# Kernel tuning notes

Hardware: AMD Instinct MI355X
Metric: run time of the kernel (lower is better)

## Reference

```python
import jax, jax.numpy as jnp
import numpy as np

B, T, I, U, O, BB = 256, 1024, 64, 256, 64, 128  # batch, seq, input, units, output, backbone_units

def lecun_tanh(x):
    return 1.7159 * jnp.tanh(0.666 * x)

def setup_inputs() -> dict:
    key = jax.random.key(0)
    ks = jax.random.split(key, 13)
    def lin(k, fan_in, fan_out):
        bound = 1.0 / np.sqrt(fan_in)
        kw, kb = jax.random.split(k)
        W = jax.random.uniform(kw, (fan_in, fan_out), jnp.float32, -bound, bound)
        b = jax.random.uniform(kb, (fan_out,), jnp.float32, -bound, bound)
        return W, b
    x = jax.random.normal(ks[0], (B, T, I), jnp.float32)
    W_bb, b_bb = lin(ks[1], I + U, BB)   # backbone Linear
    W_ff1, b_ff1 = lin(ks[2], BB, U)
    W_ff2, b_ff2 = lin(ks[3], BB, U)
    W_ta, b_ta = lin(ks[4], BB, U)       # time_a
    W_tb, b_tb = lin(ks[5], BB, U)       # time_b
    W_fc, b_fc = lin(ks[6], U, O)        # readout
    return {"x": x, "W_bb": W_bb, "b_bb": b_bb, "W_ff1": W_ff1, "b_ff1": b_ff1,
            "W_ff2": W_ff2, "b_ff2": b_ff2, "W_ta": W_ta, "b_ta": b_ta,
            "W_tb": W_tb, "b_tb": b_tb, "W_fc": W_fc, "b_fc": b_fc}

def reference(x, W_bb, b_bb, W_ff1, b_ff1, W_ff2, b_ff2, W_ta, b_ta, W_tb, b_tb, W_fc, b_fc):
    ts = jnp.float32(1.0)  # default elapsed time per step
    def step(h, xt):
        z = jnp.concatenate([xt, h], axis=-1)          # [B, I+U]
        g = lecun_tanh(z @ W_bb + b_bb)                # [B, BB]
        ff1 = jnp.tanh(g @ W_ff1 + b_ff1)              # [B, U]
        ff2 = jnp.tanh(g @ W_ff2 + b_ff2)
        t_interp = jax.nn.sigmoid((g @ W_ta + b_ta) * ts + (g @ W_tb + b_tb))
        h_new = ff1 * (1.0 - t_interp) + t_interp * ff2
        return h_new, h_new
    h0 = jnp.zeros((x.shape[0], U), x.dtype)
    h_last, hs = jax.lax.scan(step, h0, jnp.swapaxes(x, 0, 1))  # hs: [T, B, U]
    hs = jnp.swapaxes(hs, 0, 1)                                  # [B, T, U]
    out = hs @ W_fc + b_fc                                       # [B, T, O]
    return out, h_last
```

## Files before the change

### kernel.cpp

```cpp
#include <hip/hip_runtime.h>
#include <stdint.h>

#define B_ 256
#define T_ 1024
#define I_ 64
#define U_ 256
#define O_ 64
#define BB_ 128

typedef unsigned int u32;
typedef unsigned short u16;
typedef _Float16 half2_t __attribute__((ext_vector_type(2)));
typedef _Float16 f16x8 __attribute__((ext_vector_type(8)));
typedef float f32x4 __attribute__((ext_vector_type(4)));

#if defined(__has_builtin)
#if __has_builtin(__builtin_amdgcn_fdot2)
#define USE_DOT2 1
#else
#define USE_DOT2 0
#endif
#else
#define USE_DOT2 0
#endif

static __device__ __forceinline__ u32 packpair(float a, float b) {
  half2_t h; h.x = (_Float16)a; h.y = (_Float16)b;
  return __builtin_bit_cast(u32, h);
}
static __device__ __forceinline__ float unpack_lo(u32 u) {
  half2_t h = __builtin_bit_cast(half2_t, u); return (float)h.x;
}
static __device__ __forceinline__ float unpack_hi(u32 u) {
  half2_t h = __builtin_bit_cast(half2_t, u); return (float)h.y;
}
static __device__ __forceinline__ float dot2acc(u32 w, u32 z, float acc) {
#if USE_DOT2
  return __builtin_amdgcn_fdot2(__builtin_bit_cast(half2_t, w),
                                __builtin_bit_cast(half2_t, z), acc, false);
#else
  half2_t hw = __builtin_bit_cast(half2_t, w);
  half2_t hz = __builtin_bit_cast(half2_t, z);
  acc += (float)hw.x * (float)hz.x;
  acc += (float)hw.y * (float)hz.y;
  return acc;
#endif
}

template <int CTRL>
static __device__ __forceinline__ float dpp_mov_f(float v) {
  return __builtin_bit_cast(float, __builtin_amdgcn_update_dpp(
      0, __builtin_bit_cast(int, v), CTRL, 0xF, 0xF, true));
}
#define DPP_XOR1 0xB1
#define DPP_XOR2 0x4E
#define DPP_HMIR 0x141
#define DPP_MIRR 0x140

static __device__ __forceinline__ float fast_tanh(float x) {
  return 1.0f - 2.0f / (1.0f + __expf(2.0f * x));
}
static __device__ __forceinline__ float fast_sigmoid(float x) {
  return 1.0f / (1.0f + __expf(-x));
}

static __device__ __forceinline__ float rcpf(float x) {
#if defined(__has_builtin) && __has_builtin(__builtin_amdgcn_rcpf)
  return __builtin_amdgcn_rcpf(x);
#else
  return 1.0f / x;
#endif
}
static __device__ __forceinline__ float exp2fast(float x) {
#if defined(__has_builtin) && __has_builtin(__builtin_amdgcn_exp2f)
  return __builtin_amdgcn_exp2f(x);
#else
  return exp2f(x);
#endif
}

static __device__ __forceinline__ f32x4 mfma16(uint4 a, uint4 b, f32x4 c) {
  return __builtin_amdgcn_mfma_f32_16x16x32_f16(
      __builtin_bit_cast(f16x8, a), __builtin_bit_cast(f16x8, b), c, 0, 0, 0);
}

static __device__ __forceinline__ void wg_barrier() {
  asm volatile("s_waitcnt lgkmcnt(0)\n\ts_barrier" ::: "memory");
}

static __device__ __forceinline__ int swzw(int w) {
  return w ^ ((w >> 4) & 4);
}

#define LOG2E 1.44269504f

__global__ __launch_bounds__(512, 2)
void cfc_mfma(const float* __restrict__ x,
              const float* __restrict__ W_bb, const float* __restrict__ b_bb,
              const float* __restrict__ W_ff1, const float* __restrict__ b_ff1,
              const float* __restrict__ W_ff2, const float* __restrict__ b_ff2,
              const float* __restrict__ W_ta,  const float* __restrict__ b_ta,
              const float* __restrict__ W_tb,  const float* __restrict__ b_tb,
              float* __restrict__ out, u32* __restrict__ Hbuf)
{
  __shared__ __align__(16) u32 s_z[2560];
  __shared__ __align__(16) u32 s_g[1024];

  const int tid = threadIdx.x;
  const int l   = tid & 63;
  const int w   = tid >> 6;
  const int c16 = l & 15;
  const int q4  = l >> 4;
  const int odd = l & 1;
  const int row0 = blockIdx.x * 16;
  const int lr = l ^ ((l >> 4) & 1);

  uint4 wbb[10];
  {
    const int colb = w * 16 + c16;
#pragma unroll
    for (int c = 0; c < 10; ++c) {
      u32 qv[4];
#pragma unroll
      for (int q = 0; q < 4; ++q) {
        const int k0 = c * 32 + q4 * 8 + 2 * q;
        qv[q] = packpair(W_bb[(size_t)k0 * BB_ + colb],
                         W_bb[(size_t)(k0 + 1) * BB_ + colb]);
      }
      wbb[c] = make_uint4(qv[0], qv[1], qv[2], qv[3]);
    }
  }
  uint4 wff[3][2][4];
#pragma unroll
  for (int ut = 0; ut < 2; ++ut) {
    const int u = w * 32 + ut * 16 + c16;
#pragma unroll
    for (int c = 0; c < 4; ++c) {
      u32 qa[4], qb[4], qc[4];
#pragma unroll
      for (int q = 0; q < 4; ++q) {
        const int k0 = c * 32 + q4 * 8 + 2 * q;
        const size_t i0 = (size_t)k0 * U_ + u, i1 = i0 + U_;
        qa[q] = packpair(W_ff1[i0], W_ff1[i1]);
        qb[q] = packpair(W_ff2[i0], W_ff2[i1]);
        qc[q] = packpair(W_ta[i0] + W_tb[i0], W_ta[i1] + W_tb[i1]);
      }
      wff[0][ut][c] = make_uint4(qa[0], qa[1], qa[2], qa[3]);
      wff[1][ut][c] = make_uint4(qb[0], qb[1], qb[2], qb[3]);
      wff[2][ut][c] = make_uint4(qc[0], qc[1], qc[2], qc[3]);
    }
  }

  const float bgs = b_bb[w * 16 + c16] * (1.332f * LOG2E);
  float b1s[2], b2s[2], btn[2];
#pragma unroll
  for (int ut = 0; ut < 2; ++ut) {
    const int u = w * 32 + ut * 16 + c16;
    b1s[ut] = b_ff1[u] * (2.0f * LOG2E);
    b2s[ut] = b_ff2[u] * (2.0f * LOG2E);
    btn[ut] = -(b_ta[u] + b_tb[u]) * LOG2E;
  }

  const int mx = tid >> 5, px = tid & 31;
  const float* xptr = x + (size_t)(row0 + mx) * T_ * I_ + 2 * px;
  const int zxs = swzw(((px >> 4) * 64 + mx + 16 * ((px >> 2) & 3)) * 4 + (px & 3));

  const int rbase = odd ? 2 : 0;
  const int m0 = q4 * 4 + rbase, m1 = m0 + 1;
  const int pg = w * 8 + (c16 >> 1);
  const int gW = ((pg >> 4) * 64 + 16 * ((pg >> 2) & 3)) * 4 + (pg & 3)
                 + 16 * q4 + (odd ? 8 : 0);
  const int gws0 = swzw(gW), gws1 = swzw(gW + 4);
  int zws0_[2], zws1_[2]; size_t hb0_[2], hb1_[2];
#pragma unroll
  for (int ut = 0; ut < 2; ++ut) {
    const int pu = w * 16 + ut * 8 + (c16 >> 1);
    const int zW = ((2 + (pu >> 4)) * 64 + 16 * ((pu >> 2) & 3)) * 4 + (pu & 3)
                   + 16 * q4 + (odd ? 8 : 0);
    zws0_[ut] = swzw(zW);
    zws1_[ut] = swzw(zW + 4);
    hb0_[ut] = (size_t)(row0 + m0) * T_ * 128 + pu;
    hb1_[ut] = (size_t)(row0 + m1) * T_ * 128 + pu;
  }

  {
    uint4* z4w = reinterpret_cast<uint4*>(s_z);
#pragma unroll
    for (int i = tid; i < 640; i += 512) z4w[i] = make_uint4(0u, 0u, 0u, 0u);
  }
  __syncthreads();
  {
    float2 xv = *(const float2*)xptr;
    s_z[zxs] = packpair(xv.x, xv.y);
  }
  __syncthreads();

  const uint4* z4 = (const uint4*)s_z;
  const uint4* g4 = (const uint4*)s_g;

  for (int t = 0; t < T_; ++t) {
    float2 xv;
    const bool ldx = (t + 1 < T_);
    if (ldx) xv = *(const float2*)(xptr + (size_t)(t + 1) * I_);

    f32x4 aA = {0.f, 0.f, 0.f, 0.f}, aB = {0.f, 0.f, 0.f, 0.f};
#pragma unroll
    for (int c = 0; c < 10; c += 2) {
      aA = mfma16(z4[c * 64 + lr],       wbb[c],     aA);
      aB = mfma16(z4[(c + 1) * 64 + lr], wbb[c + 1], aB);
    }
    const f32x4 ab = aA + aB;

    u32 gq[4];
#pragma unroll
    for (int r = 0; r < 4; ++r) {
      const float a  = __builtin_fmaf(ab[r], 1.332f * LOG2E, bgs);
      const float rr = rcpf(exp2fast(a) + 1.0f);
      const float g  = __builtin_fmaf(rr, -3.4318f, 1.7159f);
      const float gp = dpp_mov_f<DPP_XOR1>(g);
      gq[r] = odd ? packpair(gp, g) : packpair(g, gp);
    }
    s_g[gws0] = odd ? gq[2] : gq[0];
    s_g[gws1] = odd ? gq[3] : gq[1];
    wg_barrier();

    f32x4 af[3][2];
#pragma unroll
    for (int mt = 0; mt < 3; ++mt)
#pragma unroll
      for (int ut = 0; ut < 2; ++ut)
        af[mt][ut] = (f32x4){0.f, 0.f, 0.f, 0.f};
#pragma unroll
    for (int c = 0; c < 4; ++c) {
      const uint4 ga = g4[c * 64 + lr];
#pragma unroll
      for (int mt = 0; mt < 3; ++mt)
#pragma unroll
        for (int ut = 0; ut < 2; ++ut)
          af[mt][ut] = mfma16(ga, wff[mt][ut][c], af[mt][ut]);
    }

#pragma unroll
    for (int ut = 0; ut < 2; ++ut) {
      u32 hq[4];
#pragma unroll
      for (int r = 0; r < 4; ++r) {
        const float a1 = __builtin_fmaf(af[0][ut][r], 2.0f * LOG2E, b1s[ut]);
        const float f1 = __builtin_fmaf(rcpf(exp2fast(a1) + 1.0f), -2.0f, 1.0f);
        const float a2 = __builtin_fmaf(af[1][ut][r], 2.0f * LOG2E, b2s[ut]);
        const float f2 = __builtin_fmaf(rcpf(exp2fast(a2) + 1.0f), -2.0f, 1.0f);
        const float at = __builtin_fmaf(af[2][ut][r], -LOG2E, btn[ut]);
        const float ti = rcpf(exp2fast(at) + 1.0f);
        const float h  = __builtin_fmaf(ti, f2 - f1, f1);
        const float hp = dpp_mov_f<DPP_XOR1>(h);
        hq[r] = odd ? packpair(hp, h) : packpair(h, hp);
      }
      const u32 s0 = odd ? hq[2] : hq[0];
      const u32 s1 = odd ? hq[3] : hq[1];
      s_z[zws0_[ut]] = s0;
      s_z[zws1_[ut]] = s1;
      Hbuf[hb0_[ut] + (size_t)t * 128] = s0;
      Hbuf[hb1_[ut] + (size_t)t * 128] = s1;
    }
    if (ldx) s_z[zxs] = packpair(xv.x, xv.y);
    wg_barrier();
  }

  {
    const uint4 hv = z4[128 + (tid ^ ((tid >> 4) & 1))];
    float2* tail = (float2*)(out + (size_t)B_ * T_ * O_);
#pragma unroll
    for (int i = 0; i < 4; ++i) {
      const int vh   = tid * 4 + i;
      const int ch   = vh >> 8;
      const int lane = (vh >> 2) & 63;
      const int slot = vh & 3;
      const int m    = lane & 15;
      const int bq   = lane >> 4;
      const int pu   = ch * 16 + bq * 4 + slot;
      const u32 hp   = (i == 0) ? hv.x : (i == 1) ? hv.y : (i == 2) ? hv.z : hv.w;
      float2 hf; hf.x = unpack_lo(hp); hf.y = unpack_hi(hp);
      tail[(size_t)(row0 + m) * 128 + pu] = hf;
    }
  }
}

template <bool DEFER>
__global__ __launch_bounds__(1024)
void cfc_kernel(const float* __restrict__ x,
                const float* __restrict__ W_bb, const float* __restrict__ b_bb,
                const float* __restrict__ W_ff1, const float* __restrict__ b_ff1,
                const float* __restrict__ W_ff2, const float* __restrict__ b_ff2,
                const float* __restrict__ W_ta,  const float* __restrict__ b_ta,
                const float* __restrict__ W_tb,  const float* __restrict__ b_tb,
                const float* __restrict__ W_fc,  const float* __restrict__ b_fc,
                float* __restrict__ out, u32* __restrict__ Hbuf)
{
  __shared__ __align__(16) u32 s_z2[160];
  __shared__ __align__(16) u32 s_g2[64];
  u16* s_gh = (u16*)s_g2;

  const int tid = threadIdx.x;
  const int r   = blockIdx.x;

  const int ca  = tid >> 3;
  const int kga = tid & 7;
  const int jb = tid >> 2;
  const int kq = tid & 3;
  const int ro = tid >> 4;
  const int rk = tid & 15;

  u32 wbb[20];
#pragma unroll
  for (int j = 0; j < 5; ++j)
#pragma unroll
    for (int q = 0; q < 4; ++q) {
      int p = 4 * (kga + 8 * j) + q;
      wbb[4 * j + q] = packpair(W_bb[(2 * p) * BB_ + ca],
                                W_bb[(2 * p + 1) * BB_ + ca]);
    }
  u32 wf1[16], wf2[16], wta[16], wtb[16];
#pragma unroll
  for (int j = 0; j < 4; ++j)
#pragma unroll
    for (int q = 0; q < 4; ++q) {
      int p = 4 * (kq + 4 * j) + q;
      int k0 = 2 * p, k1 = 2 * p + 1;
      wf1[4 * j + q] = packpair(W_ff1[k0 * U_ + jb], W_ff1[k1 * U_ + jb]);
      wf2[4 * j + q] = packpair(W_ff2[k0 * U_ + jb], W_ff2[k1 * U_ + jb]);
      wta[4 * j + q] = packpair(W_ta [k0 * U_ + jb], W_ta [k1 * U_ + jb]);
      wtb[4 * j + q] = packpair(W_tb [k0 * U_ + jb], W_tb [k1 * U_ + jb]);
    }
  u32 wfc[8];
  float bfo = 0.f;
  if (!DEFER) {
#pragma unroll
    for (int j = 0; j < 2; ++j)
#pragma unroll
      for (int q = 0; q < 4; ++q) {
        int p = 4 * (rk + 16 * j) + q;
        wfc[4 * j + q] = packpair(W_fc[(2 * p) * O_ + ro],
                                  W_fc[(2 * p + 1) * O_ + ro]);
      }
    bfo = b_fc[ro];
  }
  const float bbbc = b_bb[ca];
  const float b1 = b_ff1[jb], b2 = b_ff2[jb];
  const float bta = b_ta[jb], btb = b_tb[jb];

  const float* xrow = x + (size_t)r * T_ * I_;
  const size_t out_row = (size_t)r * T_ * O_;
  u32* __restrict__ hrow = DEFER ? (Hbuf + (size_t)r * T_ * (U_ / 2)) : nullptr;

  if (tid < 160) s_z2[tid] = 0u;
  __syncthreads();
  if (tid < 32) {
    float2 xv = ((const float2*)xrow)[tid];
    s_z2[tid] = packpair(xv.x, xv.y);
  }
  __syncthreads();

  for (int t = 0; t < T_; ++t) {
    float2 xv;
    const bool ldx = (tid < 32) && (t + 1 < T_);
    if (ldx) xv = ((const float2*)(xrow + (size_t)(t + 1) * I_))[tid];

    float bacc = 0.f;
#pragma unroll
    for (int j = 0; j < 5; ++j) {
      uint4 zz = *reinterpret_cast<const uint4*>(s_z2 + 4 * (kga + 8 * j));
      bacc = dot2acc(wbb[4 * j + 0], zz.x, bacc);
      bacc = dot2acc(wbb[4 * j + 1], zz.y, bacc);
      bacc = dot2acc(wbb[4 * j + 2], zz.z, bacc);
      bacc = dot2acc(wbb[4 * j + 3], zz.w, bacc);
    }
    bacc += dpp_mov_f<DPP_XOR1>(bacc);
    bacc += dpp_mov_f<DPP_XOR2>(bacc);
    bacc += dpp_mov_f<DPP_HMIR>(bacc);
    float g = 1.7159f * fast_tanh(0.666f * (bacc + bbbc));

    float racc = 0.f;
    if (!DEFER) {
#pragma unroll
      for (int j = 0; j < 2; ++j) {
        uint4 hh = *reinterpret_cast<const uint4*>(s_z2 + 32 + 4 * (rk + 16 * j));
        racc = dot2acc(wfc[4 * j + 0], hh.x, racc);
        racc = dot2acc(wfc[4 * j + 1], hh.y, racc);
        racc = dot2acc(wfc[4 * j + 2], hh.z, racc);
        racc = dot2acc(wfc[4 * j + 3], hh.w, racc);
      }
      racc += dpp_mov_f<DPP_XOR1>(racc);
      racc += dpp_mov_f<DPP_XOR2>(racc);
      racc += dpp_mov_f<DPP_HMIR>(racc);
      racc += dpp_mov_f<DPP_MIRR>(racc);
    }
    if ((tid & 7) == 0)
      s_gh[ca] = __builtin_bit_cast(u16, (_Float16)g);
    if (!DEFER && t > 0 && rk == 0)
      out[out_row + (size_t)(t - 1) * O_ + ro] = racc + bfo;
    __syncthreads();

    float a1 = 0.f, a2 = 0.f, a3 = 0.f, a4 = 0.f;
#pragma unroll
    for (int j = 0; j < 4; ++j) {
      uint4 gg = *reinterpret_cast<const uint4*>(s_g2 + 4 * (kq + 4 * j));
      a1 = dot2acc(wf1[4 * j + 0], gg.x, a1);
      a1 = dot2acc(wf1[4 * j + 1], gg.y, a1);
      a1 = dot2acc(wf1[4 * j + 2], gg.z, a1);
      a1 = dot2acc(wf1[4 * j + 3], gg.w, a1);
      a2 = dot2acc(wf2[4 * j + 0], gg.x, a2);
      a2 = dot2acc(wf2[4 * j + 1], gg.y, a2);
      a2 = dot2acc(wf2[4 * j + 2], gg.z, a2);
      a2 = dot2acc(wf2[4 * j + 3], gg.w, a2);
      a3 = dot2acc(wta[4 * j + 0], gg.x, a3);
      a3 = dot2acc(wta[4 * j + 1], gg.y, a3);
      a3 = dot2acc(wta[4 * j + 2], gg.z, a3);
      a3 = dot2acc(wta[4 * j + 3], gg.w, a3);
      a4 = dot2acc(wtb[4 * j + 0], gg.x, a4);
      a4 = dot2acc(wtb[4 * j + 1], gg.y, a4);
      a4 = dot2acc(wtb[4 * j + 2], gg.z, a4);
      a4 = dot2acc(wtb[4 * j + 3], gg.w, a4);
    }
    a1 += dpp_mov_f<DPP_XOR1>(a1); a1 += dpp_mov_f<DPP_XOR2>(a1);
    a2 += dpp_mov_f<DPP_XOR1>(a2); a2 += dpp_mov_f<DPP_XOR2>(a2);
    a3 += dpp_mov_f<DPP_XOR1>(a3); a3 += dpp_mov_f<DPP_XOR2>(a3);
    a4 += dpp_mov_f<DPP_XOR1>(a4); a4 += dpp_mov_f<DPP_XOR2>(a4);
    float f1 = fast_tanh(a1 + b1);
    float f2 = fast_tanh(a2 + b2);
    float ti = fast_sigmoid(a3 + bta + a4 + btb);
    float h  = f1 + ti * (f2 - f1);
    float hq = dpp_mov_f<DPP_HMIR>(h);

    if ((tid & 7) == 0) {
      u32 pr = packpair(h, hq);
      int m = tid >> 3;
      s_z2[32 + m] = pr;
      if (DEFER) hrow[(size_t)t * (U_ / 2) + m] = pr;
    }
    if (ldx) s_z2[tid] = packpair(xv.x, xv.y);
    __syncthreads();
  }

  if (!DEFER) {
    float racc = 0.f;
#pragma unroll
    for (int j = 0; j < 2; ++j) {
      uint4 hh = *reinterpret_cast<const uint4*>(s_z2 + 32 + 4 * (rk + 16 * j));
      racc = dot2acc(wfc[4 * j + 0], hh.x, racc);
      racc = dot2acc(wfc[4 * j + 1], hh.y, racc);
      racc = dot2acc(wfc[4 * j + 2], hh.z, racc);
      racc = dot2acc(wfc[4 * j + 3], hh.w, racc);
    }
    racc += dpp_mov_f<DPP_XOR1>(racc);
    racc += dpp_mov_f<DPP_XOR2>(racc);
    racc += dpp_mov_f<DPP_HMIR>(racc);
    racc += dpp_mov_f<DPP_MIRR>(racc);
    if (rk == 0)
      out[out_row + (size_t)(T_ - 1) * O_ + ro] = racc + bfo;
  }

  if (tid < 128) {
    u32 hp = s_z2[32 + tid];
    float2 hv; hv.x = unpack_lo(hp); hv.y = unpack_hi(hp);
    ((float2*)(out + (size_t)B_ * T_ * O_))[r * 128 + tid] = hv;
  }
}

__global__ __launch_bounds__(512)
void ro_kernel(const u32* __restrict__ Hbuf,
               const float* __restrict__ W_fc, const float* __restrict__ b_fc,
               float* __restrict__ out)
{
  __shared__ __align__(16) u32 s_h[8 * 128];
  const int tid = threadIdx.x;
  const int o   = tid & 63;
  const int w   = tid >> 6;
  const int r   = blockIdx.x;

  u32 wfc[128];
#pragma unroll
  for (int p = 0; p < 128; ++p)
    wfc[p] = packpair(W_fc[(2 * p) * O_ + o], W_fc[(2 * p + 1) * O_ + o]);
  const float bo = b_fc[o];

  const u32* hrow = Hbuf + (size_t)r * T_ * 128;
  const size_t out_row = (size_t)r * T_ * O_;

  for (int c = 0; c < T_ / 8; ++c) {
    *(uint2*)(s_h + 2 * tid) =
        *(const uint2*)(hrow + (size_t)c * 1024 + 2 * tid);
    __syncthreads();
    float acc = bo;
    const uint4* h4 = reinterpret_cast<const uint4*>(s_h + w * 128);
#pragma unroll
    for (int i = 0; i < 32; ++i) {
      uint4 hh = h4[i];
      acc = dot2acc(wfc[4 * i + 0], hh.x, acc);
      acc = dot2acc(wfc[4 * i + 1], hh.y, acc);
      acc = dot2acc(wfc[4 * i + 2], hh.z, acc);
      acc = dot2acc(wfc[4 * i + 3], hh.w, acc);
    }
    out[out_row + (size_t)(8 * c + w) * O_ + o] = acc;
    __syncthreads();
  }
}

extern "C" void kernel_launch(void* const* d_in, const int* in_sizes, int n_in,
                              void* d_out, int out_size, void* d_ws, size_t ws_size,
                              hipStream_t stream) {
  const float* x     = (const float*)d_in[0];
  const float* W_bb  = (const float*)d_in[1];
  const float* b_bb  = (const float*)d_in[2];
  const float* W_ff1 = (const float*)d_in[3];
  const float* b_ff1 = (const float*)d_in[4];
  const float* W_ff2 = (const float*)d_in[5];
  const float* b_ff2 = (const float*)d_in[6];
  const float* W_ta  = (const float*)d_in[7];
  const float* b_ta  = (const float*)d_in[8];
  const float* W_tb  = (const float*)d_in[9];
  const float* b_tb  = (const float*)d_in[10];
  const float* W_fc  = (const float*)d_in[11];
  const float* b_fc  = (const float*)d_in[12];
  float* out = (float*)d_out;

  const size_t h_bytes = (size_t)B_ * T_ * (U_ / 2) * sizeof(u32);
  if (ws_size >= h_bytes) {
    u32* Hbuf = (u32*)d_ws;
    cfc_mfma<<<dim3(B_ / 16), dim3(512), 0, stream>>>(
        x, W_bb, b_bb, W_ff1, b_ff1, W_ff2, b_ff2,
        W_ta, b_ta, W_tb, b_tb, out, Hbuf);
    ro_kernel<<<dim3(B_), dim3(512), 0, stream>>>(Hbuf, W_fc, b_fc, out);
  } else {
    cfc_kernel<false><<<dim3(B_), dim3(1024), 0, stream>>>(
        x, W_bb, b_bb, W_ff1, b_ff1, W_ff2, b_ff2,
        W_ta, b_ta, W_tb, b_tb, W_fc, b_fc, out, nullptr);
  }
}
```

Before: 1.946 ms.

## Split recurrent step across 16 waves with split-K backbone and parallel readout

The recurrent kernel moves from 8 to 16 waves per block. The backbone matmul is split in K across two wave groups, with the partial sums reduced through shared memory, and each wave now handles one 16-unit output tile instead of two. The gate math is rewritten to use a single reciprocal per element instead of three, and the readout kernel grid is split over time chunks to get more blocks. The aim is to shorten the per-step serial latency of the 16-block recurrence, at the cost of an extra barrier per step and fewer register-resident weights per wave.

```diff
diff --git a/kernel.cpp b/kernel.cpp
--- a/kernel.cpp
+++ b/kernel.cpp
@@ -94,7 +94,7 @@
 
 #define LOG2E 1.44269504f
 
-__global__ __launch_bounds__(512, 2)
+__global__ __launch_bounds__(1024, 4)
 void cfc_mfma(const float* __restrict__ x,
               const float* __restrict__ W_bb, const float* __restrict__ b_bb,
               const float* __restrict__ W_ff1, const float* __restrict__ b_ff1,
@@ -105,93 +105,85 @@
 {
   __shared__ __align__(16) u32 s_z[2560];
   __shared__ __align__(16) u32 s_g[1024];
+  __shared__ __align__(16) float s_red[2048];
 
   const int tid = threadIdx.x;
   const int l   = tid & 63;
   const int w   = tid >> 6;
+  const int wt  = w & 7;
+  const int kh  = w >> 3;
   const int c16 = l & 15;
   const int q4  = l >> 4;
   const int odd = l & 1;
   const int row0 = blockIdx.x * 16;
-  const int lr = l ^ ((l >> 4) & 1);
-
-  uint4 wbb[10];
+  const int lr  = l ^ ((l >> 4) & 1);
+
+  uint4 wbb[5];
   {
-    const int colb = w * 16 + c16;
-#pragma unroll
-    for (int c = 0; c < 10; ++c) {
+    const int colb = wt * 16 + c16;
+#pragma unroll
+    for (int c = 0; c < 5; ++c) {
+      const int kc = kh * 5 + c;
       u32 qv[4];
 #pragma unroll
       for (int q = 0; q < 4; ++q) {
-        const int k0 = c * 32 + q4 * 8 + 2 * q;
+        const int k0 = kc * 32 + q4 * 8 + 2 * q;
         qv[q] = packpair(W_bb[(size_t)k0 * BB_ + colb],
                          W_bb[(size_t)(k0 + 1) * BB_ + colb]);
       }
       wbb[c] = make_uint4(qv[0], qv[1], qv[2], qv[3]);
     }
   }
-  uint4 wff[3][2][4];
-#pragma unroll
-  for (int ut = 0; ut < 2; ++ut) {
-    const int u = w * 32 + ut * 16 + c16;
-#pragma unroll
-    for (int c = 0; c < 4; ++c) {
-      u32 qa[4], qb[4], qc[4];
-#pragma unroll
-      for (int q = 0; q < 4; ++q) {
-        const int k0 = c * 32 + q4 * 8 + 2 * q;
-        const size_t i0 = (size_t)k0 * U_ + u, i1 = i0 + U_;
-        qa[q] = packpair(W_ff1[i0], W_ff1[i1]);
-        qb[q] = packpair(W_ff2[i0], W_ff2[i1]);
-        qc[q] = packpair(W_ta[i0] + W_tb[i0], W_ta[i1] + W_tb[i1]);
-      }
-      wff[0][ut][c] = make_uint4(qa[0], qa[1], qa[2], qa[3]);
-      wff[1][ut][c] = make_uint4(qb[0], qb[1], qb[2], qb[3]);
-      wff[2][ut][c] = make_uint4(qc[0], qc[1], qc[2], qc[3]);
-    }
-  }
-
-  const float bgs = b_bb[w * 16 + c16] * (1.332f * LOG2E);
-  float b1s[2], b2s[2], btn[2];
-#pragma unroll
-  for (int ut = 0; ut < 2; ++ut) {
-    const int u = w * 32 + ut * 16 + c16;
-    b1s[ut] = b_ff1[u] * (2.0f * LOG2E);
-    b2s[ut] = b_ff2[u] * (2.0f * LOG2E);
-    btn[ut] = -(b_ta[u] + b_tb[u]) * LOG2E;
-  }
-
-  const int mx = tid >> 5, px = tid & 31;
+  uint4 wff0[4], wff1[4], wff2[4];
+  const int uu = w * 16 + c16;
+#pragma unroll
+  for (int c = 0; c < 4; ++c) {
+    u32 qa[4], qb[4], qc[4];
+#pragma unroll
+    for (int q = 0; q < 4; ++q) {
+      const int k0 = c * 32 + q4 * 8 + 2 * q;
+      const size_t i0 = (size_t)k0 * U_ + uu, i1 = i0 + U_;
+      qa[q] = packpair(W_ff1[i0], W_ff1[i1]);
+      qb[q] = packpair(W_ff2[i0], W_ff2[i1]);
+      qc[q] = packpair(W_ta[i0] + W_tb[i0], W_ta[i1] + W_tb[i1]);
+    }
+    wff0[c] = make_uint4(qa[0], qa[1], qa[2], qa[3]);
+    wff1[c] = make_uint4(qb[0], qb[1], qb[2], qb[3]);
+    wff2[c] = make_uint4(qc[0], qc[1], qc[2], qc[3]);
+  }
+
+  const float bgs = b_bb[wt * 16 + c16] * (1.332f * LOG2E);
+  const float b1s = b_ff1[uu] * (2.0f * LOG2E);
+  const float b2s = b_ff2[uu] * (2.0f * LOG2E);
+  const float btn = -(b_ta[uu] + b_tb[uu]) * LOG2E;
+
+  const int ix = tid & 511;
+  const int mx = ix >> 5, px = ix & 31;
   const float* xptr = x + (size_t)(row0 + mx) * T_ * I_ + 2 * px;
-  const int zxs = swzw(((px >> 4) * 64 + mx + 16 * ((px >> 2) & 3)) * 4 + (px & 3));
-
-  const int rbase = odd ? 2 : 0;
-  const int m0 = q4 * 4 + rbase, m1 = m0 + 1;
-  const int pg = w * 8 + (c16 >> 1);
-  const int gW = ((pg >> 4) * 64 + 16 * ((pg >> 2) & 3)) * 4 + (pg & 3)
-                 + 16 * q4 + (odd ? 8 : 0);
+  const int zxs = swzw((px >> 4) * 256 + 64 * ((px >> 2) & 3) + 4 * mx + (px & 3));
+
+  const int m0 = 4 * q4 + 2 * odd;
+  const int pg = wt * 8 + (c16 >> 1);
+  const int gW = (pg >> 4) * 256 + 64 * ((pg >> 2) & 3) + (pg & 3) + 4 * m0;
   const int gws0 = swzw(gW), gws1 = swzw(gW + 4);
-  int zws0_[2], zws1_[2]; size_t hb0_[2], hb1_[2];
-#pragma unroll
-  for (int ut = 0; ut < 2; ++ut) {
-    const int pu = w * 16 + ut * 8 + (c16 >> 1);
-    const int zW = ((2 + (pu >> 4)) * 64 + 16 * ((pu >> 2) & 3)) * 4 + (pu & 3)
-                   + 16 * q4 + (odd ? 8 : 0);
-    zws0_[ut] = swzw(zW);
-    zws1_[ut] = swzw(zW + 4);
-    hb0_[ut] = (size_t)(row0 + m0) * T_ * 128 + pu;
-    hb1_[ut] = (size_t)(row0 + m1) * T_ * 128 + pu;
-  }
+
+  const int pu = w * 8 + (c16 >> 1);
+  const int pz = 32 + pu;
+  const int zW = (pz >> 4) * 256 + 64 * ((pz >> 2) & 3) + (pz & 3) + 4 * m0;
+  const int zws0 = swzw(zW), zws1 = swzw(zW + 4);
+  const u32 hoff0 = (u32)(row0 + m0) * T_ * 128 + pu;
+  const u32 hoff1 = hoff0 + (u32)T_ * 128;
+
+  const int redw = (wt * 64 + l) * 4;
 
   {
     uint4* z4w = reinterpret_cast<uint4*>(s_z);
-#pragma unroll
-    for (int i = tid; i < 640; i += 512) z4w[i] = make_uint4(0u, 0u, 0u, 0u);
+    if (tid < 640) z4w[tid] = make_uint4(0u, 0u, 0u, 0u);
   }
   __syncthreads();
-  {
-    float2 xv = *(const float2*)xptr;
-    s_z[zxs] = packpair(xv.x, xv.y);
+  if (w >= 8) {
+    float2 x0 = *(const float2*)xptr;
+    s_z[zxs] = packpair(x0.x, x0.y);
   }
   __syncthreads();
 
@@ -200,73 +192,76 @@
 
   for (int t = 0; t < T_; ++t) {
     float2 xv;
-    const bool ldx = (t + 1 < T_);
+    const bool ldx = (w >= 8) && (t + 1 < T_);
     if (ldx) xv = *(const float2*)(xptr + (size_t)(t + 1) * I_);
 
     f32x4 aA = {0.f, 0.f, 0.f, 0.f}, aB = {0.f, 0.f, 0.f, 0.f};
-#pragma unroll
-    for (int c = 0; c < 10; c += 2) {
-      aA = mfma16(z4[c * 64 + lr],       wbb[c],     aA);
-      aB = mfma16(z4[(c + 1) * 64 + lr], wbb[c + 1], aB);
+    {
+      const int cb = kh * 5;
+      aA = mfma16(z4[(cb + 0) * 64 + lr], wbb[0], aA);
+      aB = mfma16(z4[(cb + 1) * 64 + lr], wbb[1], aB);
+      aA = mfma16(z4[(cb + 2) * 64 + lr], wbb[2], aA);
+      aB = mfma16(z4[(cb + 3) * 64 + lr], wbb[3], aB);
+      aA = mfma16(z4[(cb + 4) * 64 + lr], wbb[4], aA);
     }
     const f32x4 ab = aA + aB;
-
-    u32 gq[4];
-#pragma unroll
-    for (int r = 0; r < 4; ++r) {
-      const float a  = __builtin_fmaf(ab[r], 1.332f * LOG2E, bgs);
-      const float rr = rcpf(exp2fast(a) + 1.0f);
-      const float g  = __builtin_fmaf(rr, -3.4318f, 1.7159f);
-      const float gp = dpp_mov_f<DPP_XOR1>(g);
-      gq[r] = odd ? packpair(gp, g) : packpair(g, gp);
-    }
-    s_g[gws0] = odd ? gq[2] : gq[0];
-    s_g[gws1] = odd ? gq[3] : gq[1];
+    if (kh) *(f32x4*)(s_red + redw) = ab;
     wg_barrier();
 
-    f32x4 af[3][2];
-#pragma unroll
-    for (int mt = 0; mt < 3; ++mt)
-#pragma unroll
-      for (int ut = 0; ut < 2; ++ut)
-        af[mt][ut] = (f32x4){0.f, 0.f, 0.f, 0.f};
+    if (!kh) {
+      const f32x4 pr = *(const f32x4*)(s_red + redw);
+      u32 gq[4];
+#pragma unroll
+      for (int r = 0; r < 4; ++r) {
+        const float full = ab[r] + pr[r];
+        const float a  = __builtin_fmaf(full, 1.332f * LOG2E, bgs);
+        const float rr = rcpf(exp2fast(a) + 1.0f);
+        const float g  = __builtin_fmaf(rr, -3.4318f, 1.7159f);
+        const float gp = dpp_mov_f<DPP_XOR1>(g);
+        gq[r] = odd ? packpair(gp, g) : packpair(g, gp);
+      }
+      s_g[gws0] = odd ? gq[2] : gq[0];
+      s_g[gws1] = odd ? gq[3] : gq[1];
+    }
+    wg_barrier();
+
+    f32x4 af0 = {0.f, 0.f, 0.f, 0.f};
+    f32x4 af1 = {0.f, 0.f, 0.f, 0.f};
+    f32x4 af2 = {0.f, 0.f, 0.f, 0.f};
 #pragma unroll
     for (int c = 0; c < 4; ++c) {
       const uint4 ga = g4[c * 64 + lr];
-#pragma unroll
-      for (int mt = 0; mt < 3; ++mt)
-#pragma unroll
-        for (int ut = 0; ut < 2; ++ut)
-          af[mt][ut] = mfma16(ga, wff[mt][ut][c], af[mt][ut]);
-    }
-
-#pragma unroll
-    for (int ut = 0; ut < 2; ++ut) {
-      u32 hq[4];
-#pragma unroll
-      for (int r = 0; r < 4; ++r) {
-        const float a1 = __builtin_fmaf(af[0][ut][r], 2.0f * LOG2E, b1s[ut]);
-        const float f1 = __builtin_fmaf(rcpf(exp2fast(a1) + 1.0f), -2.0f, 1.0f);
-        const float a2 = __builtin_fmaf(af[1][ut][r], 2.0f * LOG2E, b2s[ut]);
-        const float f2 = __builtin_fmaf(rcpf(exp2fast(a2) + 1.0f), -2.0f, 1.0f);
-        const float at = __builtin_fmaf(af[2][ut][r], -LOG2E, btn[ut]);
-        const float ti = rcpf(exp2fast(at) + 1.0f);
-        const float h  = __builtin_fmaf(ti, f2 - f1, f1);
-        const float hp = dpp_mov_f<DPP_XOR1>(h);
-        hq[r] = odd ? packpair(hp, h) : packpair(h, hp);
-      }
-      const u32 s0 = odd ? hq[2] : hq[0];
-      const u32 s1 = odd ? hq[3] : hq[1];
-      s_z[zws0_[ut]] = s0;
-      s_z[zws1_[ut]] = s1;
-      Hbuf[hb0_[ut] + (size_t)t * 128] = s0;
-      Hbuf[hb1_[ut] + (size_t)t * 128] = s1;
+      af0 = mfma16(ga, wff0[c], af0);
+      af1 = mfma16(ga, wff1[c], af1);
+      af2 = mfma16(ga, wff2[c], af2);
     }
     if (ldx) s_z[zxs] = packpair(xv.x, xv.y);
+
+    u32 hq[4];
+#pragma unroll
+    for (int r = 0; r < 4; ++r) {
+      const float E1 = exp2fast(__builtin_fmaf(af0[r], 2.0f * LOG2E, b1s));
+      const float E2 = exp2fast(__builtin_fmaf(af1[r], 2.0f * LOG2E, b2s));
+      const float E3 = exp2fast(__builtin_fmaf(af2[r], -LOG2E, btn));
+      const float p2 = E2 + 1.0f, p3 = E3 + 1.0f;
+      const float qq = p2 * p3;
+      const float D  = __builtin_fmaf(E1, qq, qq);
+      const float R  = rcpf(D);
+      const float u2 = (E2 - E1) - qq;
+      const float h  = __builtin_fmaf(R + R, u2, 1.0f);
+      const float hp = dpp_mov_f<DPP_XOR1>(h);
+      hq[r] = odd ? packpair(hp, h) : packpair(h, hp);
+    }
+    const u32 s0 = odd ? hq[2] : hq[0];
+    const u32 s1 = odd ? hq[3] : hq[1];
+    s_z[zws0] = s0;
+    s_z[zws1] = s1;
+    Hbuf[hoff0 + (u32)t * 128] = s0;
+    Hbuf[hoff1 + (u32)t * 128] = s1;
     wg_barrier();
   }
 
-  {
+  if (tid < 512) {
     const uint4 hv = z4[128 + (tid ^ ((tid >> 4) & 1))];
     float2* tail = (float2*)(out + (size_t)B_ * T_ * O_);
 #pragma unroll
@@ -277,10 +272,10 @@
       const int slot = vh & 3;
       const int m    = lane & 15;
       const int bq   = lane >> 4;
-      const int pu   = ch * 16 + bq * 4 + slot;
+      const int pp   = ch * 16 + bq * 4 + slot;
       const u32 hp   = (i == 0) ? hv.x : (i == 1) ? hv.y : (i == 2) ? hv.z : hv.w;
       float2 hf; hf.x = unpack_lo(hp); hf.y = unpack_hi(hp);
-      tail[(size_t)(row0 + m) * 128 + pu] = hf;
+      tail[(size_t)(row0 + m) * 128 + pp] = hf;
     }
   }
 }
@@ -476,6 +471,7 @@
   const int o   = tid & 63;
   const int w   = tid >> 6;
   const int r   = blockIdx.x;
+  const int c0  = blockIdx.y * 16;
 
   u32 wfc[128];
 #pragma unroll
@@ -486,7 +482,7 @@
   const u32* hrow = Hbuf + (size_t)r * T_ * 128;
   const size_t out_row = (size_t)r * T_ * O_;
 
-  for (int c = 0; c < T_ / 8; ++c) {
+  for (int c = c0; c < c0 + 16; ++c) {
     *(uint2*)(s_h + 2 * tid) =
         *(const uint2*)(hrow + (size_t)c * 1024 + 2 * tid);
     __syncthreads();
@@ -526,10 +522,10 @@
   const size_t h_bytes = (size_t)B_ * T_ * (U_ / 2) * sizeof(u32);
   if (ws_size >= h_bytes) {
     u32* Hbuf = (u32*)d_ws;
-    cfc_mfma<<<dim3(B_ / 16), dim3(512), 0, stream>>>(
+    cfc_mfma<<<dim3(B_ / 16), dim3(1024), 0, stream>>>(
         x, W_bb, b_bb, W_ff1, b_ff1, W_ff2, b_ff2,
         W_ta, b_ta, W_tb, b_tb, out, Hbuf);
-    ro_kernel<<<dim3(B_), dim3(512), 0, stream>>>(Hbuf, W_fc, b_fc, out);
+    ro_kernel<<<dim3(B_, 8), dim3(512), 0, stream>>>(Hbuf, W_fc, b_fc, out);
   } else {
     cfc_kernel<false><<<dim3(B_), dim3(1024), 0, stream>>>(
         x, W_bb, b_bb, W_ff1, b_ff1, W_ff2, b_ff2,
```

Result: slower. 2.009 ms (+3.2%).
